# Optimization experiments

Hardware: AMD Instinct MI355X
Metric: run time of the kernel (lower is better)

The kernel has to match this reference:

```python
import jax, jax.numpy as jnp
import numpy as np

DIM = 512
HEADS = 8
HEAD_DIM = DIM // HEADS
B, S = 2, 4096


def rope(x):
    # x: [b, s, h, d]
    half = x.shape[-1] // 2
    freqs = 10000.0 ** (-jnp.linspace(0.0, 1.0, half, endpoint=False))  # [half]
    theta = jnp.arange(x.shape[1], dtype=jnp.float32)[None, :, None, None] * freqs[None, None, None, :]
    cos, sin = jnp.cos(theta), jnp.sin(theta)
    rx, ry = x[..., :half], x[..., half:]
    return jnp.concatenate((rx * cos - ry * sin, rx * sin + ry * cos), axis=-1)


def setup_inputs() -> dict:
    key = jax.random.key(0)
    ks = jax.random.split(key, 9)
    sd_in = 1.0 / np.sqrt(DIM)
    sd_o = 1.0 / np.sqrt(DIM)
    return {
        "x": jax.random.normal(ks[0], (B, S, DIM), jnp.float32),
        "wq_k": jax.random.normal(ks[1], (DIM, HEADS, HEAD_DIM), jnp.float32) * sd_in,
        "wq_b": jnp.zeros((HEADS, HEAD_DIM), jnp.float32),
        "wk_k": jax.random.normal(ks[2], (DIM, HEADS, HEAD_DIM), jnp.float32) * sd_in,
        "wk_b": jnp.zeros((HEADS, HEAD_DIM), jnp.float32),
        "wv_k": jax.random.normal(ks[3], (DIM, HEADS, HEAD_DIM), jnp.float32) * sd_in,
        "wv_b": jnp.zeros((HEADS, HEAD_DIM), jnp.float32),
        "wo_k": jax.random.normal(ks[4], (HEADS, HEAD_DIM, DIM), jnp.float32) * sd_o,
        "wo_b": jnp.zeros((DIM,), jnp.float32),
    }


def reference(x, wq_k, wq_b, wk_k, wk_b, wv_k, wv_b, wo_k, wo_b):
    q = rope(jnp.einsum("bsd,dhk->bshk", x, wq_k) + wq_b)
    k = rope(jnp.einsum("bsd,dhk->bshk", x, wk_k) + wk_b)
    v = jnp.einsum("bsd,dhk->bshk", x, wv_k) + wv_b
    scores = jnp.einsum("bqhd,bkhd->bhqk", q, k) / (HEAD_DIM ** 0.5)
    attn = jax.nn.softmax(scores, axis=-1)
    o = jnp.einsum("bhqk,bkhd->bqhd", attn, v)
    return jnp.einsum("bqhd,hdm->bqm", o, wo_k) + wo_b
```

## Files before the change

kernel.cpp:

```cpp
#include <hip/hip_runtime.h>

typedef __bf16 bf16x4 __attribute__((ext_vector_type(4)));
typedef __bf16 bf16x8 __attribute__((ext_vector_type(8)));
typedef float  f32x4  __attribute__((ext_vector_type(4)));

#define MFMA(a, b, c) __builtin_amdgcn_mfma_f32_16x16x32_bf16(a, b, c, 0, 0, 0)

static constexpr int kHeads = 8;
static constexpr int kS     = 4096;

#define CSC 0.18033688011112042f
#define LF  (13.287712379549449f / 32.0f)
#define INV2PI 0.15915494309189535f

__device__ inline float fexp2(float x) {
#if __has_builtin(__builtin_amdgcn_exp2f)
  return __builtin_amdgcn_exp2f(x);
#else
  return __expf(x * 0.6931471805599453f);
#endif
}
__device__ inline float fsin_rev(float rev) {
#if __has_builtin(__builtin_amdgcn_sinf)
  return __builtin_amdgcn_sinf(rev);
#else
  return __sinf(rev * 6.283185307179586f);
#endif
}
__device__ inline float fcos_rev(float rev) {
#if __has_builtin(__builtin_amdgcn_cosf)
  return __builtin_amdgcn_cosf(rev);
#else
  return __cosf(rev * 6.283185307179586f);
#endif
}

__device__ inline int perm32(int d) {
  return (((d >> 2) & 3) << 3) + (((d >> 4) & 1) << 2) + (d & 3);
}

__device__ inline void gl16(const void* src, void* lds) {
  __builtin_amdgcn_global_load_lds(
      (const __attribute__((address_space(1))) unsigned int*)src,
      (__attribute__((address_space(3))) unsigned int*)lds, 16, 0, 0);
}

__global__ __launch_bounds__(256) void wprep(
    const float* __restrict__ w0, const float* __restrict__ w1,
    const float* __restrict__ w2, __bf16* __restrict__ dstb) {
  const int kb32 = blockIdx.x, m = blockIdx.y;
  const float* W = (m == 0) ? w0 : (m == 1) ? w1 : w2;
  bf16x8* dst = (bf16x8*)dstb;
  for (int e = threadIdx.x; e < 2048; e += 256) {
    int lg = e >> 9, col = e & 511;
    bf16x8 v;
    #pragma unroll
    for (int j = 0; j < 8; ++j) {
      int k = kb32 * 32 + 4 * lg + (j & 3) + 16 * (j >> 2);
      v[j] = (__bf16)W[(size_t)k * 512 + col];
    }
    dst[(((size_t)m * 16 + kb32) * 4 + lg) * 512 + col] = v;
  }
}

__global__ __launch_bounds__(256) void qkv(
    const float* __restrict__ x, const __bf16* __restrict__ Wqkvb,
    const float* __restrict__ bq, const float* __restrict__ bk,
    const float* __restrict__ bv,
    __bf16* __restrict__ Qb, __bf16* __restrict__ Kb, __bf16* __restrict__ Vt)
{
  const int tt   = blockIdx.x;
  const int hp   = blockIdx.y;
  const int wave = threadIdx.x >> 6;
  const int lane = threadIdx.x & 63;
  const int l15  = lane & 15;
  const int lg   = lane >> 4;

  const int tok0 = tt * 64 + wave * 16;
  const float* xrow = x + (size_t)(tok0 + l15) * 512;
  const bf16x8* Wf = (const bf16x8*)Wqkvb;

  f32x4 acc[6][4];
  #pragma unroll
  for (int t = 0; t < 6; ++t)
    #pragma unroll
    for (int cb = 0; cb < 4; ++cb) acc[t][cb] = f32x4{0.f, 0.f, 0.f, 0.f};

  for (int kb32 = 0; kb32 < 16; ++kb32) {
    f32x4 xa  = *(const f32x4*)(xrow + kb32 * 32 + 4 * lg);
    f32x4 xb4 = *(const f32x4*)(xrow + kb32 * 32 + 16 + 4 * lg);
    bf16x8 af;
    af[0] = (__bf16)xa.x; af[1] = (__bf16)xa.y; af[2] = (__bf16)xa.z; af[3] = (__bf16)xa.w;
    af[4] = (__bf16)xb4.x; af[5] = (__bf16)xb4.y; af[6] = (__bf16)xb4.z; af[7] = (__bf16)xb4.w;
    #pragma unroll
    for (int t = 0; t < 6; ++t) {
      const int m = t >> 1, hh = t & 1;
      const int colb = (hp * 2 + hh) * 64;
      const bf16x8* wrow = Wf + (((size_t)m * 16 + kb32) * 4 + lg) * 512 + colb + l15;
      #pragma unroll
      for (int cb = 0; cb < 4; ++cb)
        acc[t][cb] = MFMA(af, wrow[cb * 16], acc[t][cb]);
    }
  }

  const float frrev0 = fexp2(-LF * (float)l15) * INV2PI;
  const float frrev1 = fexp2(-LF * (float)(16 + l15)) * INV2PI;
  float snv[4][2], csv[4][2];
  #pragma unroll
  for (int r = 0; r < 4; ++r) {
    float sp = (float)((tok0 + 4 * lg + r) & (kS - 1));
    #pragma unroll
    for (int cb = 0; cb < 2; ++cb) {
      float rev = sp * (cb == 0 ? frrev0 : frrev1);
      rev -= floorf(rev);
      snv[r][cb] = fsin_rev(rev);
      csv[r][cb] = fcos_rev(rev);
    }
  }

  #pragma unroll
  for (int t = 0; t < 6; ++t) {
    const int m = t >> 1, hh = t & 1;
    const int h = hp * 2 + hh;
    const float* bias = (m == 0) ? bq : (m == 1) ? bk : bv;
    #pragma unroll
    for (int cb = 0; cb < 4; ++cb) {
      float bv_ = bias[h * 64 + cb * 16 + l15];
      #pragma unroll
      for (int r = 0; r < 4; ++r) acc[t][cb][r] += bv_;
    }
    if (m < 2) {
      #pragma unroll
      for (int r = 0; r < 4; ++r)
        #pragma unroll
        for (int cb = 0; cb < 2; ++cb) {
          float rx = acc[t][cb][r], ry = acc[t][cb + 2][r];
          acc[t][cb][r]     = rx * csv[r][cb] - ry * snv[r][cb];
          acc[t][cb + 2][r] = rx * snv[r][cb] + ry * csv[r][cb];
        }
      if (m == 0) {
        #pragma unroll
        for (int cb = 0; cb < 4; ++cb)
          #pragma unroll
          for (int r = 0; r < 4; ++r) acc[t][cb][r] *= CSC;
      }
    }
    #pragma unroll
    for (int r = 0; r < 4; ++r) {
      int tok = tok0 + 4 * lg + r;
      int b = tok >> 12, srow = tok & (kS - 1);
      size_t bh = (size_t)(b * kHeads + h);
      #pragma unroll
      for (int cb = 0; cb < 4; ++cb) {
        int d = cb * 16 + l15;
        __bf16 v = (__bf16)acc[t][cb][r];
        if (m < 2) {
          int slot = (d & ~31) + perm32(d & 31);
          if (m == 0) Qb[(bh * kS + srow) * 64 + slot] = v;
          else        Kb[(bh * kS + srow) * 64 + slot] = v;
        } else {
          Vt[((size_t)bh * 64 + d) * kS + (srow & ~31) + perm32(srow & 31)] = v;
        }
      }
    }
  }
}

__global__ __launch_bounds__(512) void attn(
    const __bf16* __restrict__ Qb, const __bf16* __restrict__ Kb,
    const __bf16* __restrict__ Vt, __bf16* __restrict__ Ob)
{
  __shared__ __align__(16) char smem[49152];

  const int id   = blockIdx.x;
  const int bh   = ((id & 7) << 1) | ((id >> 3) & 1);
  const int qt   = id >> 4;
  const int tid  = threadIdx.x;
  const int wave = tid >> 6;
  const int lane = tid & 63;
  const int l15  = lane & 15;
  const int lg   = lane >> 4;

  const __bf16* Qp = Qb + (size_t)bh * kS * 64;
  const char*   Kp = (const char*)(Kb + (size_t)bh * kS * 64);
  const char*   Vp = (const char*)(Vt + (size_t)bh * 64 * kS);

  const int q0 = qt * 128 + wave * 16;

  bf16x8 qf[2];
  #pragma unroll
  for (int dh = 0; dh < 2; ++dh)
    qf[dh] = *(const bf16x8*)(Qp + (size_t)(q0 + l15) * 64 + dh * 32 + 8 * lg);

  const int srow = tid >> 3;
  const int ssw  = ((tid & 7) * 16) ^ ((srow & 7) << 4);
  const char* ksrc = Kp + (size_t)srow * 128 + ssw;
  const char* vsrc = Vp + (size_t)srow * 8192 + ssw;
  const int   kdst = wave * 1024;
  const int   vdst = 8192 + wave * 1024;

  const int swz = (l15 & 7) << 4;
  const int ka0 = l15 * 128 + ((16 * lg) ^ swz);
  const int ka1 = l15 * 128 + ((64 + 16 * lg) ^ swz);
  const int va0 = 8192 + ka0;
  const int va1 = 8192 + ka1;

  const f32x4 kZero = f32x4{0.f, 0.f, 0.f, 0.f};

  char* const B0 = smem;
  char* const B1 = smem + 16384;
  char* const B2 = smem + 32768;

  f32x4 oacc[4];
  #pragma unroll
  for (int db = 0; db < 4; ++db) oacc[db] = kZero;
  float lp = 0.f;
  bf16x8 paP[2], paC[2];

  gl16(ksrc, B0 + kdst);
  gl16(vsrc, B0 + vdst);
  ksrc += 8192; vsrc += 128;
  __syncthreads();
  gl16(ksrc, B1 + kdst);
  gl16(vsrc, B1 + vdst);
  ksrc += 8192; vsrc += 128;
  {
    f32x4 sa[4];
    __builtin_amdgcn_s_setprio(1);
    #pragma unroll
    for (int kh = 0; kh < 4; ++kh) {
      bf16x8 kf0 = *(const bf16x8*)(B0 + kh * 2048 + ka0);
      bf16x8 kf1 = *(const bf16x8*)(B0 + kh * 2048 + ka1);
      sa[kh] = MFMA(kf0, qf[0], kZero);
      sa[kh] = MFMA(kf1, qf[1], sa[kh]);
    }
    __builtin_amdgcn_s_setprio(0);
    #pragma unroll
    for (int kh = 0; kh < 4; ++kh)
      #pragma unroll
      for (int rr = 0; rr < 4; ++rr) {
        float p = fexp2(sa[kh][rr]);
        lp += p;
        paP[kh >> 1][(kh & 1) * 4 + rr] = (__bf16)p;
      }
  }

  auto body = [&](const char* sbP, const char* sbC, char* sbN, bool doStage) {
    __syncthreads();
    if (doStage) {
      gl16(ksrc, sbN + kdst);
      gl16(vsrc, sbN + vdst);
      ksrc += 8192; vsrc += 128;
    }
    f32x4 sa[4];
    __builtin_amdgcn_s_setprio(1);
    #pragma unroll
    for (int kh = 0; kh < 4; ++kh) {
      bf16x8 kf0 = *(const bf16x8*)(sbC + kh * 2048 + ka0);
      bf16x8 kf1 = *(const bf16x8*)(sbC + kh * 2048 + ka1);
      sa[kh] = MFMA(kf0, qf[0], kZero);
      sa[kh] = MFMA(kf1, qf[1], sa[kh]);
    }
    #pragma unroll
    for (int db = 0; db < 4; ++db) {
      bf16x8 vf0 = *(const bf16x8*)(sbP + db * 2048 + va0);
      bf16x8 vf1 = *(const bf16x8*)(sbP + db * 2048 + va1);
      oacc[db] = MFMA(vf0, paP[0], oacc[db]);
      oacc[db] = MFMA(vf1, paP[1], oacc[db]);
    }
    __builtin_amdgcn_s_setprio(0);
    #pragma unroll
    for (int kh = 0; kh < 4; ++kh)
      #pragma unroll
      for (int rr = 0; rr < 4; ++rr) {
        float p = fexp2(sa[kh][rr]);
        lp += p;
        paC[kh >> 1][(kh & 1) * 4 + rr] = (__bf16)p;
      }
    paP[0] = paC[0];
    paP[1] = paC[1];
  };

  for (int g = 0; g < 20; ++g) {
    body(B0, B1, B2, true);
    body(B1, B2, B0, true);
    body(B2, B0, B1, true);
  }
  body(B0, B1, B2, true);
  body(B1, B2, B0, true);
  body(B2, B0, B1, false);

  {
    __builtin_amdgcn_s_setprio(1);
    #pragma unroll
    for (int db = 0; db < 4; ++db) {
      bf16x8 vf0 = *(const bf16x8*)(B0 + db * 2048 + va0);
      bf16x8 vf1 = *(const bf16x8*)(B0 + db * 2048 + va1);
      oacc[db] = MFMA(vf0, paP[0], oacc[db]);
      oacc[db] = MFMA(vf1, paP[1], oacc[db]);
    }
    __builtin_amdgcn_s_setprio(0);
  }

  float lrun = lp;
  lrun += __shfl_xor(lrun, 16);
  lrun += __shfl_xor(lrun, 32);
  float inv = 1.0f / lrun;

  const int b = bh >> 3, h = bh & 7;
  const int q = q0 + l15;
  #pragma unroll
  for (int db = 0; db < 4; ++db) {
    bf16x4 o4;
    #pragma unroll
    for (int rr = 0; rr < 4; ++rr) o4[rr] = (__bf16)(oacc[db][rr] * inv);
    size_t e = ((size_t)(b * kS + q)) * 512 + h * 64 + (db >> 1) * 32 + 8 * lg + 4 * (db & 1);
    *(bf16x4*)(Ob + e) = o4;
  }
}

__global__ __launch_bounds__(256) void oproj(
    const __bf16* __restrict__ Ob, const __bf16* __restrict__ Wofb,
    const float* __restrict__ wob, float* __restrict__ out)
{
  const int tt   = blockIdx.x;
  const int ct   = blockIdx.y;
  const int wave = threadIdx.x >> 6;
  const int lane = threadIdx.x & 63;
  const int l15  = lane & 15;
  const int lg   = lane >> 4;

  const int tok0 = tt * 64 + wave * 16;
  const int colbase = ct * 64;
  const __bf16* orow = Ob + (size_t)(tok0 + l15) * 512;
  const bf16x8* Wf = (const bf16x8*)Wofb;

  f32x4 acc[4];
  #pragma unroll
  for (int cb = 0; cb < 4; ++cb) acc[cb] = f32x4{0.f, 0.f, 0.f, 0.f};

  for (int kb32 = 0; kb32 < 16; ++kb32) {
    bf16x8 af = *(const bf16x8*)(orow + kb32 * 32 + 8 * lg);
    const bf16x8* wrow = Wf + ((size_t)kb32 * 4 + lg) * 512 + colbase + l15;
    #pragma unroll
    for (int cb = 0; cb < 4; ++cb)
      acc[cb] = MFMA(af, wrow[cb * 16], acc[cb]);
  }

  #pragma unroll
  for (int cb = 0; cb < 4; ++cb) {
    int col = colbase + cb * 16 + l15;
    float bv_ = wob[col];
    #pragma unroll
    for (int r = 0; r < 4; ++r) {
      int tok = tok0 + 4 * lg + r;
      out[(size_t)tok * 512 + col] = acc[cb][r] + bv_;
    }
  }
}

extern "C" void kernel_launch(void* const* d_in, const int* in_sizes, int n_in,
                              void* d_out, int out_size, void* d_ws, size_t ws_size,
                              hipStream_t stream)
{
  const float* x   = (const float*)d_in[0];
  const float* wq  = (const float*)d_in[1];
  const float* bq  = (const float*)d_in[2];
  const float* wk  = (const float*)d_in[3];
  const float* bk  = (const float*)d_in[4];
  const float* wv  = (const float*)d_in[5];
  const float* bv  = (const float*)d_in[6];
  const float* wo  = (const float*)d_in[7];
  const float* wob = (const float*)d_in[8];
  float* out = (float*)d_out;

  const size_t n = (size_t)8192 * 512;
  __bf16* Qb   = (__bf16*)d_ws;
  __bf16* Kb   = Qb + n;
  __bf16* Vt   = Kb + n;
  __bf16* Ob   = Vt + n;
  __bf16* Wqkv = Ob;
  __bf16* Wof  = Qb;

  wprep<<<dim3(16, 3), 256, 0, stream>>>(wq, wk, wv, Wqkv);
  qkv<<<dim3(128, 4), 256, 0, stream>>>(x, Wqkv, bq, bk, bv, Qb, Kb, Vt);
  attn<<<512, 512, 0, stream>>>(Qb, Kb, Vt, Ob);
  wprep<<<dim3(16, 1), 256, 0, stream>>>(wo, wo, wo, Wof);
  oproj<<<dim3(128, 8), 256, 0, stream>>>(Ob, Wof, wob, out);
}
```

Before: 136.2 us.

## Stage QKV weight tiles through double-buffered LDS with async global-to-LDS loads

The QKV projection kernel now loads each k-slice of packed bf16 weights into a double-buffered 48KB shared-memory region using gl16 (likely direct global-to-LDS copies), prefetching the next slice while MFMAs consume the current one. Previously every wave read the same weight fragments straight from global memory. The change is meant to cut redundant global/L2 weight traffic across the four waves and hide load latency. The cost is a block barrier per iteration and extra LDS use, which may lower occupancy.

```diff
diff --git a/kernel.cpp b/kernel.cpp
--- a/kernel.cpp
+++ b/kernel.cpp
@@ -69,16 +69,30 @@
     const float* __restrict__ bv,
     __bf16* __restrict__ Qb, __bf16* __restrict__ Kb, __bf16* __restrict__ Vt)
 {
+  __shared__ __align__(16) char wsm[49152];
+
   const int tt   = blockIdx.x;
   const int hp   = blockIdx.y;
-  const int wave = threadIdx.x >> 6;
-  const int lane = threadIdx.x & 63;
+  const int tid  = threadIdx.x;
+  const int wave = tid >> 6;
+  const int lane = tid & 63;
   const int l15  = lane & 15;
   const int lg   = lane >> 4;
 
   const int tok0 = tt * 64 + wave * 16;
   const float* xrow = x + (size_t)(tok0 + l15) * 512;
-  const bf16x8* Wf = (const bf16x8*)Wqkvb;
+  const char*  Wc   = (const char*)Wqkvb;
+
+  const char* wsrc[6];
+  #pragma unroll
+  for (int c = 0; c < 6; ++c) {
+    int idx  = c * 256 + tid;
+    int m    = idx >> 9;
+    int lgw  = (idx >> 7) & 3;
+    int colr = idx & 127;
+    wsrc[c] = Wc + ((((size_t)m * 16 + 0) * 4 + lgw) * 512 + hp * 128 + colr) * 16;
+  }
+  const int wdst = wave * 1024;
 
   f32x4 acc[6][4];
   #pragma unroll
@@ -86,21 +100,38 @@
     #pragma unroll
     for (int cb = 0; cb < 4; ++cb) acc[t][cb] = f32x4{0.f, 0.f, 0.f, 0.f};
 
+  #pragma unroll
+  for (int c = 0; c < 6; ++c)
+    gl16(wsrc[c], wsm + c * 4096 + wdst);
+
+  int buf = 0;
   for (int kb32 = 0; kb32 < 16; ++kb32) {
+    __syncthreads();
+    if (kb32 + 1 < 16) {
+      char* sb = wsm + ((buf ^ 1) ? 24576 : 0);
+      #pragma unroll
+      for (int c = 0; c < 6; ++c)
+        gl16(wsrc[c] + (size_t)(kb32 + 1) * 32768, sb + c * 4096 + wdst);
+    }
+    const char* sb = wsm + (buf ? 24576 : 0);
+
     f32x4 xa  = *(const f32x4*)(xrow + kb32 * 32 + 4 * lg);
     f32x4 xb4 = *(const f32x4*)(xrow + kb32 * 32 + 16 + 4 * lg);
     bf16x8 af;
     af[0] = (__bf16)xa.x; af[1] = (__bf16)xa.y; af[2] = (__bf16)xa.z; af[3] = (__bf16)xa.w;
     af[4] = (__bf16)xb4.x; af[5] = (__bf16)xb4.y; af[6] = (__bf16)xb4.z; af[7] = (__bf16)xb4.w;
+
     #pragma unroll
     for (int t = 0; t < 6; ++t) {
       const int m = t >> 1, hh = t & 1;
-      const int colb = (hp * 2 + hh) * 64;
-      const bf16x8* wrow = Wf + (((size_t)m * 16 + kb32) * 4 + lg) * 512 + colb + l15;
-      #pragma unroll
-      for (int cb = 0; cb < 4; ++cb)
-        acc[t][cb] = MFMA(af, wrow[cb * 16], acc[t][cb]);
-    }
+      const char* wb = sb + m * 8192 + lg * 2048 + (hh * 64 + l15) * 16;
+      #pragma unroll
+      for (int cb = 0; cb < 4; ++cb) {
+        bf16x8 w = *(const bf16x8*)(wb + cb * 256);
+        acc[t][cb] = MFMA(af, w, acc[t][cb]);
+      }
+    }
+    buf ^= 1;
   }
 
   const float frrev0 = fexp2(-LF * (float)l15) * INV2PI;
```

Measured after the change: 154.5 us. 1.13x slower.

## Process two 16-row query tiles per wave in attention, halving block threads

Applied to the files above, without the earlier changes.

Each attention wave now handles 32 query rows (two 16-row MFMA tiles) instead of 16, so every K and V fragment read from shared memory feeds two MFMAs. The block shrinks from 512 to 256 threads, and each thread stages two K rows and two V rows per tile to keep the same 64-key tile in LDS. This is meant to halve LDS reads per unit of MFMA work and cut barrier participants. The cost is doubled per-thread accumulator and probability registers and half as many waves for hiding latency.

```diff
diff --git a/kernel.cpp b/kernel.cpp
--- a/kernel.cpp
+++ b/kernel.cpp
@@ -166,7 +166,7 @@
   }
 }
 
-__global__ __launch_bounds__(512) void attn(
+__global__ __launch_bounds__(256) void attn(
     const __bf16* __restrict__ Qb, const __bf16* __restrict__ Kb,
     const __bf16* __restrict__ Vt, __bf16* __restrict__ Ob)
 {
@@ -185,19 +185,21 @@
   const char*   Kp = (const char*)(Kb + (size_t)bh * kS * 64);
   const char*   Vp = (const char*)(Vt + (size_t)bh * 64 * kS);
 
-  const int q0 = qt * 128 + wave * 16;
-
-  bf16x8 qf[2];
-  #pragma unroll
-  for (int dh = 0; dh < 2; ++dh)
-    qf[dh] = *(const bf16x8*)(Qp + (size_t)(q0 + l15) * 64 + dh * 32 + 8 * lg);
-
-  const int srow = tid >> 3;
-  const int ssw  = ((tid & 7) * 16) ^ ((srow & 7) << 4);
-  const char* ksrc = Kp + (size_t)srow * 128 + ssw;
-  const char* vsrc = Vp + (size_t)srow * 8192 + ssw;
-  const int   kdst = wave * 1024;
-  const int   vdst = 8192 + wave * 1024;
+  const int q0 = qt * 128 + wave * 32;
+
+  bf16x8 qf[2][2];
+  #pragma unroll
+  for (int qi = 0; qi < 2; ++qi)
+    #pragma unroll
+    for (int dh = 0; dh < 2; ++dh)
+      qf[qi][dh] = *(const bf16x8*)(Qp + (size_t)(q0 + qi * 16 + l15) * 64 + dh * 32 + 8 * lg);
+
+  const int r0 = tid >> 3, c0 = tid & 7, r1 = r0 + 32;
+  const char* ksrc0 = Kp + (size_t)r0 * 128 + ((16 * c0) ^ ((r0 & 7) << 4));
+  const char* ksrc1 = Kp + (size_t)r1 * 128 + ((16 * c0) ^ ((r1 & 7) << 4));
+  const char* vsrc0 = Vp + (size_t)r0 * 8192 + ((16 * c0) ^ ((r0 & 7) << 4));
+  const char* vsrc1 = Vp + (size_t)r1 * 8192 + ((16 * c0) ^ ((r1 & 7) << 4));
+  const int wb = wave * 1024;
 
   const int swz = (l15 & 7) << 4;
   const int ka0 = l15 * 128 + ((16 * lg) ^ swz);
@@ -211,74 +213,90 @@
   char* const B1 = smem + 16384;
   char* const B2 = smem + 32768;
 
-  f32x4 oacc[4];
-  #pragma unroll
-  for (int db = 0; db < 4; ++db) oacc[db] = kZero;
-  float lp = 0.f;
-  bf16x8 paP[2], paC[2];
-
-  gl16(ksrc, B0 + kdst);
-  gl16(vsrc, B0 + vdst);
-  ksrc += 8192; vsrc += 128;
+  f32x4 oacc[2][4];
+  #pragma unroll
+  for (int qi = 0; qi < 2; ++qi)
+    #pragma unroll
+    for (int db = 0; db < 4; ++db) oacc[qi][db] = kZero;
+  float lp0 = 0.f, lp1 = 0.f;
+  bf16x8 paP[2][2], paC[2][2];
+
+  auto stage = [&](char* sb) {
+    gl16(ksrc0, sb + wb);          gl16(ksrc1, sb + 4096 + wb);
+    gl16(vsrc0, sb + 8192 + wb);   gl16(vsrc1, sb + 12288 + wb);
+    ksrc0 += 8192; ksrc1 += 8192; vsrc0 += 128; vsrc1 += 128;
+  };
+
+  stage(B0);
   __syncthreads();
-  gl16(ksrc, B1 + kdst);
-  gl16(vsrc, B1 + vdst);
-  ksrc += 8192; vsrc += 128;
+  stage(B1);
   {
-    f32x4 sa[4];
+    f32x4 sa[2][4];
     __builtin_amdgcn_s_setprio(1);
     #pragma unroll
     for (int kh = 0; kh < 4; ++kh) {
       bf16x8 kf0 = *(const bf16x8*)(B0 + kh * 2048 + ka0);
       bf16x8 kf1 = *(const bf16x8*)(B0 + kh * 2048 + ka1);
-      sa[kh] = MFMA(kf0, qf[0], kZero);
-      sa[kh] = MFMA(kf1, qf[1], sa[kh]);
+      #pragma unroll
+      for (int qi = 0; qi < 2; ++qi) {
+        sa[qi][kh] = MFMA(kf0, qf[qi][0], kZero);
+        sa[qi][kh] = MFMA(kf1, qf[qi][1], sa[qi][kh]);
+      }
     }
     __builtin_amdgcn_s_setprio(0);
     #pragma unroll
-    for (int kh = 0; kh < 4; ++kh)
-      #pragma unroll
-      for (int rr = 0; rr < 4; ++rr) {
-        float p = fexp2(sa[kh][rr]);
-        lp += p;
-        paP[kh >> 1][(kh & 1) * 4 + rr] = (__bf16)p;
-      }
+    for (int qi = 0; qi < 2; ++qi)
+      #pragma unroll
+      for (int kh = 0; kh < 4; ++kh)
+        #pragma unroll
+        for (int rr = 0; rr < 4; ++rr) {
+          float p = fexp2(sa[qi][kh][rr]);
+          if (qi == 0) lp0 += p; else lp1 += p;
+          paP[qi][kh >> 1][(kh & 1) * 4 + rr] = (__bf16)p;
+        }
   }
 
   auto body = [&](const char* sbP, const char* sbC, char* sbN, bool doStage) {
     __syncthreads();
-    if (doStage) {
-      gl16(ksrc, sbN + kdst);
-      gl16(vsrc, sbN + vdst);
-      ksrc += 8192; vsrc += 128;
-    }
-    f32x4 sa[4];
+    if (doStage) stage(sbN);
+    f32x4 sa[2][4];
     __builtin_amdgcn_s_setprio(1);
     #pragma unroll
     for (int kh = 0; kh < 4; ++kh) {
       bf16x8 kf0 = *(const bf16x8*)(sbC + kh * 2048 + ka0);
       bf16x8 kf1 = *(const bf16x8*)(sbC + kh * 2048 + ka1);
-      sa[kh] = MFMA(kf0, qf[0], kZero);
-      sa[kh] = MFMA(kf1, qf[1], sa[kh]);
+      #pragma unroll
+      for (int qi = 0; qi < 2; ++qi) {
+        sa[qi][kh] = MFMA(kf0, qf[qi][0], kZero);
+        sa[qi][kh] = MFMA(kf1, qf[qi][1], sa[qi][kh]);
+      }
     }
     #pragma unroll
     for (int db = 0; db < 4; ++db) {
       bf16x8 vf0 = *(const bf16x8*)(sbP + db * 2048 + va0);
       bf16x8 vf1 = *(const bf16x8*)(sbP + db * 2048 + va1);
-      oacc[db] = MFMA(vf0, paP[0], oacc[db]);
-      oacc[db] = MFMA(vf1, paP[1], oacc[db]);
+      #pragma unroll
+      for (int qi = 0; qi < 2; ++qi) {
+        oacc[qi][db] = MFMA(vf0, paP[qi][0], oacc[qi][db]);
+        oacc[qi][db] = MFMA(vf1, paP[qi][1], oacc[qi][db]);
+      }
     }
     __builtin_amdgcn_s_setprio(0);
     #pragma unroll
-    for (int kh = 0; kh < 4; ++kh)
-      #pragma unroll
-      for (int rr = 0; rr < 4; ++rr) {
-        float p = fexp2(sa[kh][rr]);
-        lp += p;
-        paC[kh >> 1][(kh & 1) * 4 + rr] = (__bf16)p;
-      }
-    paP[0] = paC[0];
-    paP[1] = paC[1];
+    for (int qi = 0; qi < 2; ++qi)
+      #pragma unroll
+      for (int kh = 0; kh < 4; ++kh)
+        #pragma unroll
+        for (int rr = 0; rr < 4; ++rr) {
+          float p = fexp2(sa[qi][kh][rr]);
+          if (qi == 0) lp0 += p; else lp1 += p;
+          paC[qi][kh >> 1][(kh & 1) * 4 + rr] = (__bf16)p;
+        }
+    #pragma unroll
+    for (int qi = 0; qi < 2; ++qi) {
+      paP[qi][0] = paC[qi][0];
+      paP[qi][1] = paC[qi][1];
+    }
   };
 
   for (int g = 0; g < 20; ++g) {
@@ -296,26 +314,31 @@
     for (int db = 0; db < 4; ++db) {
       bf16x8 vf0 = *(const bf16x8*)(B0 + db * 2048 + va0);
       bf16x8 vf1 = *(const bf16x8*)(B0 + db * 2048 + va1);
-      oacc[db] = MFMA(vf0, paP[0], oacc[db]);
-      oacc[db] = MFMA(vf1, paP[1], oacc[db]);
+      #pragma unroll
+      for (int qi = 0; qi < 2; ++qi) {
+        oacc[qi][db] = MFMA(vf0, paP[qi][0], oacc[qi][db]);
+        oacc[qi][db] = MFMA(vf1, paP[qi][1], oacc[qi][db]);
+      }
     }
     __builtin_amdgcn_s_setprio(0);
   }
 
-  float lrun = lp;
-  lrun += __shfl_xor(lrun, 16);
-  lrun += __shfl_xor(lrun, 32);
-  float inv = 1.0f / lrun;
-
   const int b = bh >> 3, h = bh & 7;
-  const int q = q0 + l15;
-  #pragma unroll
-  for (int db = 0; db < 4; ++db) {
-    bf16x4 o4;
-    #pragma unroll
-    for (int rr = 0; rr < 4; ++rr) o4[rr] = (__bf16)(oacc[db][rr] * inv);
-    size_t e = ((size_t)(b * kS + q)) * 512 + h * 64 + (db >> 1) * 32 + 8 * lg + 4 * (db & 1);
-    *(bf16x4*)(Ob + e) = o4;
+  #pragma unroll
+  for (int qi = 0; qi < 2; ++qi) {
+    float lrun = (qi == 0) ? lp0 : lp1;
+    lrun += __shfl_xor(lrun, 16);
+    lrun += __shfl_xor(lrun, 32);
+    float inv = 1.0f / lrun;
+    const int q = q0 + qi * 16 + l15;
+    #pragma unroll
+    for (int db = 0; db < 4; ++db) {
+      bf16x4 o4;
+      #pragma unroll
+      for (int rr = 0; rr < 4; ++rr) o4[rr] = (__bf16)(oacc[qi][db][rr] * inv);
+      size_t e = ((size_t)(b * kS + q)) * 512 + h * 64 + (db >> 1) * 32 + 8 * lg + 4 * (db & 1);
+      *(bf16x4*)(Ob + e) = o4;
+    }
   }
 }
 
@@ -384,7 +407,7 @@
 
   wprep<<<dim3(16, 3), 256, 0, stream>>>(wq, wk, wv, Wqkv);
   qkv<<<dim3(128, 4), 256, 0, stream>>>(x, Wqkv, bq, bk, bv, Qb, Kb, Vt);
-  attn<<<512, 512, 0, stream>>>(Qb, Kb, Vt, Ob);
+  attn<<<512, 256, 0, stream>>>(Qb, Kb, Vt, Ob);
   wprep<<<dim3(16, 1), 256, 0, stream>>>(wo, wo, wo, Wof);
   oproj<<<dim3(128, 8), 256, 0, stream>>>(Ob, Wof, wob, out);
 }
```

Result: slower. 143.6 us (+5.4%).
